# Performance work log

Hardware: AMD Instinct MI355X
Metric: run time of the kernel (lower is better)

## Reference

```python
import jax, jax.numpy as jnp
import numpy as np

V, E, HT, HC = 30000, 300, 256, 256
B, LC, T = 32, 32, 64
NTAG = 9  # output_dim + 2


def lstm_dir(x, lens, Wih, Whh, b, reverse):
    """Variable-length single-direction LSTM (packed-sequence semantics).
    x: [N, T, D], lens: [N] int. Returns outputs [N, T, H] zeroed at pad steps.
    Masked state update keeps h,c frozen at pad steps, so reverse=True starts
    from each sequence's true last element (zeros carry through leading pads).
    """
    N, Tn, _ = x.shape
    H = Whh.shape[1]
    gx = jnp.einsum('ntd,gd->ntg', x, Wih) + b            # [N,T,4H]
    mask = jnp.arange(Tn)[None, :] < lens[:, None]         # [N,T]

    def step(carry, inp):
        h, c = carry
        g_t, m = inp                                       # [N,4H], [N]
        gates = g_t + h @ Whh.T
        i, f, g, o = jnp.split(gates, 4, axis=-1)
        c_new = jax.nn.sigmoid(f) * c + jax.nn.sigmoid(i) * jnp.tanh(g)
        h_new = jax.nn.sigmoid(o) * jnp.tanh(c_new)
        m = m[:, None]
        h2 = jnp.where(m, h_new, h)
        c2 = jnp.where(m, c_new, c)
        return (h2, c2), jnp.where(m, h2, 0.0)

    init = (jnp.zeros((N, H), x.dtype), jnp.zeros((N, H), x.dtype))
    xs = (jnp.swapaxes(gx, 0, 1), mask.T)
    _, ys = jax.lax.scan(step, init, xs, reverse=reverse)
    return jnp.swapaxes(ys, 0, 1)                          # [N,T,H]


def bilstm(x, lens, Wih_f, Whh_f, b_f, Wih_b, Whh_b, b_b):
    hf = lstm_dir(x, lens, Wih_f, Whh_f, b_f, reverse=False)
    hb = lstm_dir(x, lens, Wih_b, Whh_b, b_b, reverse=True)
    return jnp.concatenate([hf, hb], axis=-1)


def setup_inputs() -> dict:
    key = jax.random.key(0)
    ks = jax.random.split(key, 20)
    s = 0.05
    inp = {
        'x': jax.random.randint(ks[0], (B, LC, T), 0, V, dtype=jnp.int32),
        'x_feats': jax.random.normal(ks[1], (B, LC, 64), jnp.float32),
        'x_len': jnp.maximum(jax.random.randint(ks[2], (B,), 0, LC, dtype=jnp.int32), 1),
        'x_chunk_len': jax.random.randint(ks[3], (B, LC), 1, T + 1, dtype=jnp.int32),
        'emb': jax.random.normal(ks[4], (V, E), jnp.float32) * s,
        'tok_Wih_f': jax.random.normal(ks[5], (4 * HT, E), jnp.float32) * s,
        'tok_Whh_f': jax.random.normal(ks[6], (4 * HT, HT), jnp.float32) * s,
        'tok_b_f': jax.random.normal(ks[7], (4 * HT,), jnp.float32) * s,
        'tok_Wih_b': jax.random.normal(ks[8], (4 * HT, E), jnp.float32) * s,
        'tok_Whh_b': jax.random.normal(ks[9], (4 * HT, HT), jnp.float32) * s,
        'tok_b_b': jax.random.normal(ks[10], (4 * HT,), jnp.float32) * s,
        'chk_Wih_f': jax.random.normal(ks[11], (4 * HC, 2 * HT), jnp.float32) * s,
        'chk_Whh_f': jax.random.normal(ks[12], (4 * HC, HC), jnp.float32) * s,
        'chk_b_f': jax.random.normal(ks[13], (4 * HC,), jnp.float32) * s,
        'chk_Wih_b': jax.random.normal(ks[14], (4 * HC, 2 * HT), jnp.float32) * s,
        'chk_Whh_b': jax.random.normal(ks[15], (4 * HC, HC), jnp.float32) * s,
        'chk_b_b': jax.random.normal(ks[16], (4 * HC,), jnp.float32) * s,
        'fc_W': jax.random.normal(ks[17], (NTAG, 2 * HC), jnp.float32) * s,
        'fc_b': jax.random.normal(ks[18], (NTAG,), jnp.float32) * s,
    }
    return inp


def reference(x, x_feats, x_len, x_chunk_len, emb,
              tok_Wih_f, tok_Whh_f, tok_b_f, tok_Wih_b, tok_Whh_b, tok_b_b,
              chk_Wih_f, chk_Whh_f, chk_b_f, chk_Wih_b, chk_Whh_b, chk_b_b,
              fc_W, fc_b):
    b, lc, t = x.shape
    xe = emb[x].reshape(b * lc, t, -1)                     # [B*LC, T, E]
    clens = jnp.clip(x_chunk_len.reshape(-1), 1, t)        # [B*LC]
    h = bilstm(xe, clens, tok_Wih_f, tok_Whh_f, tok_b_f,
               tok_Wih_b, tok_Whh_b, tok_b_b)              # [B*LC, T, 2HT]
    # gather output at last valid timestep (= [fwd final, bwd one-step])
    last = h[jnp.arange(b * lc), clens - 1]                # [B*LC, 2HT]
    chunks = last.reshape(b, lc, -1)                       # [B, LC, 2HT]
    ch = bilstm(chunks, x_len, chk_Wih_f, chk_Whh_f, chk_b_f,
                chk_Wih_b, chk_Whh_b, chk_b_b)             # [B, LC, 2HC]
    # pad_packed(total_length=LC) gives zeros at pad -> fc sees zeros there
    out = ch @ fc_W.T + fc_b                               # [B, LC, NTAG]
    return out
```

## Files before the change

### kernel.cpp

```cpp
#include <hip/hip_runtime.h>


typedef __attribute__((ext_vector_type(8))) short s16x8;
typedef __attribute__((ext_vector_type(4))) float f32x4;
typedef __attribute__((ext_vector_type(2))) unsigned int u32x2;

__device__ __forceinline__ unsigned short f2bf(float f) {
  unsigned u = __builtin_bit_cast(unsigned, f);
  u += 0x7fff + ((u >> 16) & 1);
  return (unsigned short)(u >> 16);
}
__device__ __forceinline__ float bf2f(unsigned short h) {
  unsigned u = ((unsigned)h) << 16;
  return __builtin_bit_cast(float, u);
}
__device__ __forceinline__ float sigm(float x) { return 1.f / (1.f + __expf(-x)); }
__device__ __forceinline__ float tanh_(float x) { return 1.f - 2.f / (__expf(2.f * x) + 1.f); }

union PK8 { s16x8 v; unsigned short u[8]; };

__global__ void prep_weights(const float* __restrict__ wihf, const float* __restrict__ wihb,
                             const float* __restrict__ wcf, const float* __restrict__ wcb,
                             unsigned short* __restrict__ o_wf, unsigned short* __restrict__ o_wb,
                             unsigned short* __restrict__ o_wcf, unsigned short* __restrict__ o_wcb) {
  const int job = blockIdx.y, r = blockIdx.x, tid = threadIdx.x;
  const float* src; unsigned short* dst; int Ks, Kd;
  switch (job) {
    case 0: src = wihf; dst = o_wf;   Ks = 300; Kd = 320; break;
    case 1: src = wihb; dst = o_wb;   Ks = 300; Kd = 320; break;
    case 2: src = wcf;  dst = o_wcf;  Ks = 512; Kd = 512; break;
    default:src = wcb;  dst = o_wcb;  Ks = 512; Kd = 512; break;
  }
  for (int c = tid; c < Kd; c += 256)
    dst[r * Kd + c] = f2bf(c < Ks ? src[r * Ks + c] : 0.f);
}

__global__ __launch_bounds__(256)
void prep_whh_frag(const float* __restrict__ w0, const float* __restrict__ w1,
                   const float* __restrict__ w2,
                   unsigned short* __restrict__ o0, unsigned short* __restrict__ o1,
                   unsigned short* __restrict__ o2) {
  const float* src = blockIdx.y == 0 ? w0 : (blockIdx.y == 1 ? w1 : w2);
  unsigned short* dst = blockIdx.y == 0 ? o0 : (blockIdx.y == 1 ? o1 : o2);
  const int fid = blockIdx.x;
  const int b = fid & 1, g = (fid >> 1) & 3, kt = (fid >> 3) & 7, js = fid >> 6;
  for (int i = threadIdx.x; i < 512; i += 256) {
    const int lane = i >> 3, e = i & 7;
    const int cc = lane & 15, qq = lane >> 4;
    const int row = g * 256 + (js * 2 + b) * 16 + cc;
    const int col = kt * 32 + qq * 8 + e;
    dst[(size_t)fid * 512 + i] = f2bf(src[row * 256 + col]);
  }
}

__global__ void prep_small(const int* __restrict__ x, const int* __restrict__ xcl,
                           int* __restrict__ clens, int* __restrict__ lastv,
                           int* __restrict__ order, int* __restrict__ glen) {
  __shared__ int start[65];
  const int n = threadIdx.x;
  if (n < 65) start[n] = 0;
  __syncthreads();
  int len = xcl[n]; len = len < 1 ? 1 : (len > 64 ? 64 : len);
  clens[n] = len;
  lastv[n] = x[n * 64 + len - 1];
  atomicAdd(&start[len], 1);
  __syncthreads();
  if (n == 0) {
    int acc = 0;
    for (int l = 64; l >= 1; --l) { int h = start[l]; start[l] = acc; acc += h; }
  }
  __syncthreads();
  int pos = atomicAdd(&start[len], 1);
  order[pos] = n;
  __syncthreads();
  if (n < 64) glen[n] = clens[order[n * 16]];
}

__global__ __launch_bounds__(256, 2)
void gemm_bf(const float* __restrict__ A, const int* __restrict__ rowmap,
             int Mrows, int Astride, int Klog, int KP,
             const unsigned short* __restrict__ B, unsigned short* __restrict__ C) {
  __shared__ unsigned short As[128 * 40];
  __shared__ unsigned short Ep[4][64 * 136];
  const int tid = threadIdx.x;
  const int lane = tid & 63, w = tid >> 6;
  const int wrow = w >> 1, wcol = w & 1;
  const int cc = lane & 15, qq = lane >> 4;
  const int m0 = blockIdx.y * 128, n0 = blockIdx.x * 256;

  f32x4 zz = {0.f, 0.f, 0.f, 0.f};
  f32x4 acc[4][8];
#pragma unroll
  for (int i = 0; i < 4; ++i)
#pragma unroll
    for (int j = 0; j < 8; ++j) acc[i][j] = zz;

  const int arow = tid >> 1, ahalf = tid & 1;
  const float* arp = nullptr;
  {
    int av = m0 + arow;
    if (av < Mrows) {
      int amap = rowmap ? rowmap[av] : av;
      arp = A + (long)amap * Astride;
    }
  }

  const int nktiles = KP >> 5;
  for (int kt = 0; kt < nktiles; ++kt) {
    const int k0 = kt << 5;
    __syncthreads();
    {
      const int kb = k0 + ahalf * 16;
      unsigned short hv[16];
      if (arp && kb + 16 <= Klog) {
        const float* p = arp + kb;
#pragma unroll
        for (int i = 0; i < 16; i += 4) {
          f32x4 t = *(const f32x4*)(p + i);
          hv[i] = f2bf(t.x); hv[i + 1] = f2bf(t.y);
          hv[i + 2] = f2bf(t.z); hv[i + 3] = f2bf(t.w);
        }
      } else {
#pragma unroll
        for (int i = 0; i < 16; ++i) {
          float v = (arp && (kb + i) < Klog) ? arp[kb + i] : 0.f;
          hv[i] = f2bf(v);
        }
      }
      PK8 p0, p1;
#pragma unroll
      for (int i = 0; i < 8; ++i) { p0.u[i] = hv[i]; p1.u[i] = hv[8 + i]; }
      *(s16x8*)&As[arow * 40 + ahalf * 16] = p0.v;
      *(s16x8*)&As[arow * 40 + ahalf * 16 + 8] = p1.v;
    }
    __syncthreads();
    s16x8 af[4];
#pragma unroll
    for (int mt = 0; mt < 4; ++mt)
      af[mt] = *(const s16x8*)&As[(wrow * 64 + mt * 16 + cc) * 40 + qq * 8];
#pragma unroll
    for (int nt = 0; nt < 8; ++nt) {
      const unsigned short* bp = B + (long)(n0 + wcol * 128 + nt * 16 + cc) * KP + k0 + qq * 8;
      s16x8 bfr = *(const s16x8*)bp;
#pragma unroll
      for (int mt = 0; mt < 4; ++mt)
        acc[mt][nt] = __builtin_amdgcn_mfma_f32_16x16x32_bf16(af[mt], bfr, acc[mt][nt], 0, 0, 0);
    }
  }
  __syncthreads();
#pragma unroll
  for (int mt = 0; mt < 4; ++mt)
#pragma unroll
    for (int nt = 0; nt < 8; ++nt)
#pragma unroll
      for (int r = 0; r < 4; ++r)
        Ep[w][(mt * 16 + qq * 4 + r) * 136 + nt * 16 + cc] = f2bf(acc[mt][nt][r]);
  __syncthreads();
#pragma unroll
  for (int it = 0; it < 16; ++it) {
    int row = it * 4 + qq;
    s16x8 d = *(const s16x8*)&Ep[w][row * 136 + cc * 8];
    int gm = m0 + wrow * 64 + row;
    int gn = n0 + wcol * 128 + cc * 8;
    if (gm < Mrows) *(s16x8*)&C[(long)gm * 1024 + gn] = d;
  }
}

__global__ void bwd_step(const unsigned short* __restrict__ gxb,
                         const float* __restrict__ bias,
                         float* __restrict__ chunks) {
  const int n = blockIdx.x, j = threadIdx.x;
  const unsigned short* row = gxb + (long)n * 1024;
  float gi = bf2f(row[j]) + bias[j];
  float gg = bf2f(row[512 + j]) + bias[512 + j];
  float go = bf2f(row[768 + j]) + bias[768 + j];
  float cn = sigm(gi) * tanh_(gg);
  chunks[(long)n * 512 + 256 + j] = sigm(go) * tanh_(cn);
}

__global__ __launch_bounds__(256)
void gather_gx(const unsigned short* __restrict__ proj, const int* __restrict__ x,
               const int* __restrict__ order, const int* __restrict__ clens,
               const int* __restrict__ glen, const float* __restrict__ bias,
               unsigned short* __restrict__ gx) {
  const int t = blockIdx.x, p = blockIdx.y, j = threadIdx.x;
  if (t >= glen[p >> 4]) return;
  const int seq = order[p];
  const int len = clens[seq];
  unsigned short* dst = gx + (((size_t)(p >> 4) * 64 + t) * 16 + (p & 15)) * 1024 + j * 4;
  if (t >= len) { u32x2 z = {0u, 0u}; *(u32x2*)dst = z; return; }
  const int tok = x[seq * 64 + t];
  const unsigned short* src = proj + (size_t)tok * 1024 + j;
  unsigned v0 = f2bf(bf2f(src[0]) + bias[j]);
  unsigned v1 = f2bf(bf2f(src[256]) + bias[256 + j]);
  unsigned v2 = f2bf(bf2f(src[512]) + bias[512 + j]);
  unsigned v3 = f2bf(bf2f(src[768]) + bias[768 + j]);
  u32x2 pk = {v0 | (v1 << 16), v2 | (v3 << 16)};
  *(u32x2*)dst = pk;
}

__global__ __launch_bounds__(256)
void repack4(const unsigned short* __restrict__ s0, const unsigned short* __restrict__ s1,
             const float* __restrict__ b0, const float* __restrict__ b1,
             unsigned short* __restrict__ d0, unsigned short* __restrict__ d1) {
  const int r = blockIdx.x, j = threadIdx.x;
  const int m = r >> 5, t = r & 31;
  const int mg = m >> 4, m16 = m & 15;
  const unsigned short* s = (blockIdx.y ? s1 : s0) + (size_t)r * 1024;
  const float* bb = blockIdx.y ? b1 : b0;
  unsigned short* d = (blockIdx.y ? d1 : d0) +
                      (size_t)((mg * 32 + t) * 16 + m16) * 1024 + j * 4;
  unsigned v0 = f2bf(bf2f(s[j]) + bb[j]);
  unsigned v1 = f2bf(bf2f(s[256 + j]) + bb[256 + j]);
  unsigned v2 = f2bf(bf2f(s[512 + j]) + bb[512 + j]);
  unsigned v3 = f2bf(bf2f(s[768 + j]) + bb[768 + j]);
  u32x2 pk = {v0 | (v1 << 16), v2 | (v3 << 16)};
  *(u32x2*)d = pk;
}

__global__ __launch_bounds__(1024, 4)
void tok_fwd(const unsigned short* __restrict__ gx,
             const unsigned short* __restrict__ WhP,
             const int* __restrict__ order,
             const int* __restrict__ clens,
             const int* __restrict__ glen,
             float* __restrict__ chunks) {
  extern __shared__ unsigned short smem[];
  unsigned short* hly = smem;
  unsigned short* ldsW = smem + 4224;
  int* sg = (int*)(smem + 69760);
  int* slen = sg + 16;

  const int tid = threadIdx.x;
  const int lane = tid & 63, w = tid >> 6;
  const int cc = lane & 15, qq = lane >> 4;
  const int gb = blockIdx.x;

  if (tid < 16) {
    int s = order[gb * 16 + tid];
    sg[tid] = s;
    slen[tid] = clens[s];
  }
  for (int i = tid; i < 4224; i += 1024) hly[i] = 0;

  const unsigned short* wgl = WhP + ((size_t)(w >> 1) * 64 + (w & 1)) * 512 + lane * 8;
  {
    unsigned short* ld = ldsW + w * 4096 + lane * 8;
#pragma unroll
    for (int kt = 0; kt < 2; ++kt)
#pragma unroll
      for (int g = 0; g < 4; ++g)
        *(s16x8*)&ld[(kt * 4 + g) * 512] = *(const s16x8*)&wgl[(kt * 8 + g * 2) * 512];
  }
  s16x8 Rw[4];
#pragma unroll
  for (int g = 0; g < 4; ++g) Rw[g] = *(const s16x8*)&wgl[(16 + g * 2) * 512];

  __syncthreads();

  const int maxlen = glen[gb];
  const int j = w * 16 + cc;
  int lenr[4];
#pragma unroll
  for (int r = 0; r < 4; ++r) lenr[r] = slen[qq * 4 + r];

  float cst[4];
#pragma unroll
  for (int r = 0; r < 4; ++r) cst[r] = 0.f;

  const unsigned short* gx0 = gx + (size_t)gb * 64 * 16 * 1024 + j * 4;
  const unsigned short* ldw = ldsW + w * 4096 + lane * 8;
  f32x4 zz = {0.f, 0.f, 0.f, 0.f};

  for (int t = 0; t < maxlen; ++t) {
    __syncthreads();

    u32x2 gxp[4];
#pragma unroll
    for (int r = 0; r < 4; ++r) {
      const int m = qq * 4 + r;
      gxp[r] = *(const u32x2*)(gx0 + ((size_t)t * 16 + m) * 1024);
    }

    f32x4 acc[4];
#pragma unroll
    for (int g = 0; g < 4; ++g) acc[g] = zz;

#pragma unroll
    for (int kt = 0; kt < 2; ++kt) {
      s16x8 a0 = *(const s16x8*)&hly[cc * 264 + kt * 32 + qq * 8];
#pragma unroll
      for (int g = 0; g < 4; ++g) {
        s16x8 bf = *(const s16x8*)&ldw[(kt * 4 + g) * 512];
        acc[g] = __builtin_amdgcn_mfma_f32_16x16x32_bf16(a0, bf, acc[g], 0, 0, 0);
      }
    }
    {
      s16x8 a0 = *(const s16x8*)&hly[cc * 264 + 2 * 32 + qq * 8];
#pragma unroll
      for (int g = 0; g < 4; ++g)
        acc[g] = __builtin_amdgcn_mfma_f32_16x16x32_bf16(a0, Rw[g], acc[g], 0, 0, 0);
    }
#pragma unroll 1
    for (int kt = 3; kt < 8; ++kt) {
      s16x8 Sb[4];
#pragma unroll
      for (int g = 0; g < 4; ++g)
        Sb[g] = *(const s16x8*)&wgl[(kt * 8 + g * 2) * 512];
      s16x8 a0 = *(const s16x8*)&hly[cc * 264 + kt * 32 + qq * 8];
#pragma unroll
      for (int g = 0; g < 4; ++g)
        acc[g] = __builtin_amdgcn_mfma_f32_16x16x32_bf16(a0, Sb[g], acc[g], 0, 0, 0);
    }

    __syncthreads();

#pragma unroll
    for (int r = 0; r < 4; ++r) {
      const int m = qq * 4 + r;
      const u32x2 pk = gxp[r];
      float gi = acc[0][r] + bf2f((unsigned short)(pk.x & 0xffff));
      float gf = acc[1][r] + bf2f((unsigned short)(pk.x >> 16));
      float gg = acc[2][r] + bf2f((unsigned short)(pk.y & 0xffff));
      float go = acc[3][r] + bf2f((unsigned short)(pk.y >> 16));
      if (t < lenr[r]) {
        float cn = sigm(gf) * cst[r] + sigm(gi) * tanh_(gg);
        cst[r] = cn;
        float hn = sigm(go) * tanh_(cn);
        hly[m * 264 + j] = f2bf(hn);
      }
    }
  }

  __syncthreads();
#pragma unroll
  for (int r = 0; r < 4; ++r) {
    const int m = qq * 4 + r;
    chunks[(size_t)sg[m] * 512 + j] = bf2f(hly[m * 264 + j]);
  }
}

__global__ __launch_bounds__(1024, 4)
void chunk_rec(const unsigned short* __restrict__ gxf,
               const unsigned short* __restrict__ gxb,
               const unsigned short* __restrict__ WhPf,
               const unsigned short* __restrict__ WhPb,
               const int* __restrict__ xlen,
               unsigned short* __restrict__ ch) {
  extern __shared__ unsigned short smem[];
  unsigned short* hly = smem;
  unsigned short* ldsW = smem + 4224;

  const int tid = threadIdx.x;
  const int lane = tid & 63, w = tid >> 6;
  const int cc = lane & 15, qq = lane >> 4;
  const int dir = blockIdx.x & 1, mg = blockIdx.x >> 1;
  const unsigned short* gx = (dir ? gxb : gxf) + (size_t)mg * 32 * 16 * 1024;
  const unsigned short* WhP = dir ? WhPb : WhPf;

  for (int i = tid; i < 4224; i += 1024) hly[i] = 0;

  const unsigned short* wgl = WhP + ((size_t)(w >> 1) * 64 + (w & 1)) * 512 + lane * 8;
  {
    unsigned short* ld = ldsW + w * 4096 + lane * 8;
#pragma unroll
    for (int kt = 0; kt < 2; ++kt)
#pragma unroll
      for (int g = 0; g < 4; ++g)
        *(s16x8*)&ld[(kt * 4 + g) * 512] = *(const s16x8*)&wgl[(kt * 8 + g * 2) * 512];
  }
  s16x8 Rw[4];
#pragma unroll
  for (int g = 0; g < 4; ++g) Rw[g] = *(const s16x8*)&wgl[(16 + g * 2) * 512];

  __syncthreads();

  const int j = w * 16 + cc;
  int lenr[4];
#pragma unroll
  for (int r = 0; r < 4; ++r) {
    int L = xlen[mg * 16 + qq * 4 + r];
    lenr[r] = L > 32 ? 32 : L;
  }

  float cst[4];
#pragma unroll
  for (int r = 0; r < 4; ++r) cst[r] = 0.f;

  const unsigned short* ldw = ldsW + w * 4096 + lane * 8;
  f32x4 zz = {0.f, 0.f, 0.f, 0.f};

  for (int tt = 0; tt < 32; ++tt) {
    const int t = dir ? (31 - tt) : tt;

    __syncthreads();

    u32x2 gxp[4];
#pragma unroll
    for (int r = 0; r < 4; ++r) {
      const int m = qq * 4 + r;
      gxp[r] = *(const u32x2*)(gx + ((size_t)t * 16 + m) * 1024 + j * 4);
    }

    f32x4 acc[4];
#pragma unroll
    for (int g = 0; g < 4; ++g) acc[g] = zz;

#pragma unroll
    for (int kt = 0; kt < 2; ++kt) {
      s16x8 a0 = *(const s16x8*)&hly[cc * 264 + kt * 32 + qq * 8];
#pragma unroll
      for (int g = 0; g < 4; ++g) {
        s16x8 bf = *(const s16x8*)&ldw[(kt * 4 + g) * 512];
        acc[g] = __builtin_amdgcn_mfma_f32_16x16x32_bf16(a0, bf, acc[g], 0, 0, 0);
      }
    }
    {
      s16x8 a0 = *(const s16x8*)&hly[cc * 264 + 2 * 32 + qq * 8];
#pragma unroll
      for (int g = 0; g < 4; ++g)
        acc[g] = __builtin_amdgcn_mfma_f32_16x16x32_bf16(a0, Rw[g], acc[g], 0, 0, 0);
    }
#pragma unroll 1
    for (int kt = 3; kt < 8; ++kt) {
      s16x8 Sb[4];
#pragma unroll
      for (int g = 0; g < 4; ++g)
        Sb[g] = *(const s16x8*)&wgl[(kt * 8 + g * 2) * 512];
      s16x8 a0 = *(const s16x8*)&hly[cc * 264 + kt * 32 + qq * 8];
#pragma unroll
      for (int g = 0; g < 4; ++g)
        acc[g] = __builtin_amdgcn_mfma_f32_16x16x32_bf16(a0, Sb[g], acc[g], 0, 0, 0);
    }

    __syncthreads();

#pragma unroll
    for (int r = 0; r < 4; ++r) {
      const int m = qq * 4 + r;
      const u32x2 pk = gxp[r];
      float gi = acc[0][r] + bf2f((unsigned short)(pk.x & 0xffff));
      float gf = acc[1][r] + bf2f((unsigned short)(pk.x >> 16));
      float gg = acc[2][r] + bf2f((unsigned short)(pk.y & 0xffff));
      float go = acc[3][r] + bf2f((unsigned short)(pk.y >> 16));
      unsigned short hb16 = 0;
      if (t < lenr[r]) {
        float cn = sigm(gf) * cst[r] + sigm(gi) * tanh_(gg);
        cst[r] = cn;
        float hn = sigm(go) * tanh_(cn);
        hb16 = f2bf(hn);
        hly[m * 264 + j] = hb16;
      }
      ch[(size_t)((mg * 16 + m) * 32 + t) * 512 + dir * 256 + j] = hb16;
    }
  }
}

__global__ __launch_bounds__(64)
void fc_kernel(const unsigned short* __restrict__ ch, const float* __restrict__ W,
               const float* __restrict__ bfc, float* __restrict__ out) {
  const int n = blockIdx.x, lane = threadIdx.x;
  float xv[8];
  const unsigned short* cp = ch + (long)n * 512 + lane * 8;
#pragma unroll
  for (int i = 0; i < 8; ++i) xv[i] = bf2f(cp[i]);
  float s[9];
#pragma unroll
  for (int k = 0; k < 9; ++k) {
    const float* wr = W + k * 512 + lane * 8;
    float t = 0.f;
#pragma unroll
    for (int i = 0; i < 8; ++i) t += xv[i] * wr[i];
    s[k] = t;
  }
#pragma unroll
  for (int off = 32; off; off >>= 1)
#pragma unroll
    for (int k = 0; k < 9; ++k) s[k] += __shfl_down(s[k], off, 64);
  if (lane == 0) {
#pragma unroll
    for (int k = 0; k < 9; ++k) out[n * 9 + k] = s[k] + bfc[k];
  }
}

extern "C" void kernel_launch(void* const* d_in, const int* in_sizes, int n_in,
                              void* d_out, int out_size, void* d_ws, size_t ws_size,
                              hipStream_t stream) {
  const int*   x           = (const int*)d_in[0];
  const int*   x_len       = (const int*)d_in[2];
  const int*   x_chunk_len = (const int*)d_in[3];
  const float* emb         = (const float*)d_in[4];
  const float* tok_Wih_f   = (const float*)d_in[5];
  const float* tok_Whh_f   = (const float*)d_in[6];
  const float* tok_b_f     = (const float*)d_in[7];
  const float* tok_Wih_b   = (const float*)d_in[8];
  const float* tok_b_b     = (const float*)d_in[10];
  const float* chk_Wih_f   = (const float*)d_in[11];
  const float* chk_Whh_f   = (const float*)d_in[12];
  const float* chk_b_f     = (const float*)d_in[13];
  const float* chk_Wih_b   = (const float*)d_in[14];
  const float* chk_Whh_b   = (const float*)d_in[15];
  const float* chk_b_b     = (const float*)d_in[16];
  const float* fc_W        = (const float*)d_in[17];
  const float* fc_b        = (const float*)d_in[18];
  float* out = (float*)d_out;

  char* ws = (char*)d_ws;
  size_t off = 0;
  auto alloc = [&](size_t bytes) -> void* {
    void* p = ws + off;
    off += (bytes + 255) & ~(size_t)255;
    return p;
  };
  unsigned short* Wf   = (unsigned short*)alloc((size_t)1024 * 320 * 2);
  unsigned short* Wb   = (unsigned short*)alloc((size_t)1024 * 320 * 2);
  unsigned short* Wcf  = (unsigned short*)alloc((size_t)1024 * 512 * 2);
  unsigned short* Wcb  = (unsigned short*)alloc((size_t)1024 * 512 * 2);
  unsigned short* WhPtok=(unsigned short*)alloc((size_t)512 * 512 * 2);
  unsigned short* WhPcf= (unsigned short*)alloc((size_t)512 * 512 * 2);
  unsigned short* WhPcb= (unsigned short*)alloc((size_t)512 * 512 * 2);
  unsigned short* proj = (unsigned short*)alloc((size_t)30000 * 1024 * 2);
  unsigned short* gxbb = (unsigned short*)alloc((size_t)1024 * 1024 * 2);
  unsigned short* gxcf = (unsigned short*)alloc((size_t)1024 * 1024 * 2);
  unsigned short* gxcb = (unsigned short*)alloc((size_t)1024 * 1024 * 2);
  unsigned short* gxcfp= (unsigned short*)alloc((size_t)1024 * 1024 * 2);
  unsigned short* gxcbp= (unsigned short*)alloc((size_t)1024 * 1024 * 2);
  float*          chunks = (float*)alloc((size_t)1024 * 512 * 4);
  unsigned short* cho  = (unsigned short*)alloc((size_t)1024 * 512 * 2);
  unsigned short* gxs  = (unsigned short*)alloc((size_t)1024 * 64 * 1024 * 2);
  int* clens = (int*)alloc(1024 * 4);
  int* lastv = (int*)alloc(1024 * 4);
  int* order = (int*)alloc(1024 * 4);
  int* glen  = (int*)alloc(64 * 4);

  hipFuncSetAttribute((const void*)tok_fwd,
                      hipFuncAttributeMaxDynamicSharedMemorySize, 139776);
  hipFuncSetAttribute((const void*)chunk_rec,
                      hipFuncAttributeMaxDynamicSharedMemorySize, 139520);

  prep_weights<<<dim3(1024, 4), 256, 0, stream>>>(
      tok_Wih_f, tok_Wih_b, chk_Wih_f, chk_Wih_b, Wf, Wb, Wcf, Wcb);
  prep_whh_frag<<<dim3(512, 3), 256, 0, stream>>>(
      tok_Whh_f, chk_Whh_f, chk_Whh_b, WhPtok, WhPcf, WhPcb);
  prep_small<<<1, 1024, 0, stream>>>(x, x_chunk_len, clens, lastv, order, glen);

  gemm_bf<<<dim3(4, 235), 256, 0, stream>>>(emb, nullptr, 30000, 300, 300, 320, Wf, proj);
  gemm_bf<<<dim3(4, 8), 256, 0, stream>>>(emb, lastv, 1024, 300, 300, 320, Wb, gxbb);
  bwd_step<<<1024, 256, 0, stream>>>(gxbb, tok_b_b, chunks);
  gather_gx<<<dim3(64, 1024), 256, 0, stream>>>(proj, x, order, clens, glen, tok_b_f, gxs);
  tok_fwd<<<64, 1024, 139776, stream>>>(gxs, WhPtok, order, clens, glen, chunks);
  gemm_bf<<<dim3(4, 8), 256, 0, stream>>>(chunks, nullptr, 1024, 512, 512, 512, Wcf, gxcf);
  gemm_bf<<<dim3(4, 8), 256, 0, stream>>>(chunks, nullptr, 1024, 512, 512, 512, Wcb, gxcb);
  repack4<<<dim3(1024, 2), 256, 0, stream>>>(gxcf, gxcb, chk_b_f, chk_b_b, gxcfp, gxcbp);
  chunk_rec<<<4, 1024, 139520, stream>>>(gxcfp, gxcbp, WhPcf, WhPcb, x_len, cho);
  fc_kernel<<<1024, 64, 0, stream>>>(cho, fc_W, fc_b, out);
}
```

Measured before the change: 908.3 us.

## Double-buffer hidden state in LDS and pipeline recurrent weight loads

The recurrent kernels now keep two hidden-state buffers in LDS, alternating by step. This removes one block-wide barrier per timestep. The weight sections streamed from global memory are double-buffered in registers, so the next section (and the first section of the next step) is loaded while the current one feeds the MFMAs. This costs extra LDS and register pressure. Masked rows leave stale data in the inactive buffer, which is handled by reading the final state from the buffer selected by sequence-length parity.

```diff
diff --git a/kernel.cpp b/kernel.cpp
--- a/kernel.cpp
+++ b/kernel.cpp
@@ -18,6 +18,20 @@
 __device__ __forceinline__ float tanh_(float x) { return 1.f - 2.f / (__expf(2.f * x) + 1.f); }
 
 union PK8 { s16x8 v; unsigned short u[8]; };
+
+#define LOADSEC(buf, kt) { _Pragma("unroll") \
+  for (int g = 0; g < 4; ++g) buf[g] = *(const s16x8*)&wgl[((kt) * 8 + g * 2) * 512]; }
+
+#define MFMASEC(kt, buf) { \
+  s16x8 a0 = *(const s16x8*)&hc[cc * 264 + (kt) * 32 + qq * 8]; \
+  _Pragma("unroll") for (int g = 0; g < 4; ++g) \
+    acc[g] = __builtin_amdgcn_mfma_f32_16x16x32_bf16(a0, buf[g], acc[g], 0, 0, 0); }
+
+#define MFMALDS(kt) { \
+  s16x8 a0 = *(const s16x8*)&hc[cc * 264 + (kt) * 32 + qq * 8]; \
+  _Pragma("unroll") for (int g = 0; g < 4; ++g) { \
+    s16x8 bf = *(const s16x8*)&ldw[((kt) * 4 + g) * 512]; \
+    acc[g] = __builtin_amdgcn_mfma_f32_16x16x32_bf16(a0, bf, acc[g], 0, 0, 0); } }
 
 __global__ void prep_weights(const float* __restrict__ wihf, const float* __restrict__ wihb,
                              const float* __restrict__ wcf, const float* __restrict__ wcb,
@@ -227,8 +241,8 @@
              float* __restrict__ chunks) {
   extern __shared__ unsigned short smem[];
   unsigned short* hly = smem;
-  unsigned short* ldsW = smem + 4224;
-  int* sg = (int*)(smem + 69760);
+  unsigned short* ldsW = smem + 8448;
+  int* sg = (int*)(smem + 73984);
   int* slen = sg + 16;
 
   const int tid = threadIdx.x;
@@ -241,7 +255,7 @@
     sg[tid] = s;
     slen[tid] = clens[s];
   }
-  for (int i = tid; i < 4224; i += 1024) hly[i] = 0;
+  for (int i = tid; i < 8448; i += 1024) hly[i] = 0;
 
   const unsigned short* wgl = WhP + ((size_t)(w >> 1) * 64 + (w & 1)) * 512 + lane * 8;
   {
@@ -252,9 +266,6 @@
       for (int g = 0; g < 4; ++g)
         *(s16x8*)&ld[(kt * 4 + g) * 512] = *(const s16x8*)&wgl[(kt * 8 + g * 2) * 512];
   }
-  s16x8 Rw[4];
-#pragma unroll
-  for (int g = 0; g < 4; ++g) Rw[g] = *(const s16x8*)&wgl[(16 + g * 2) * 512];
 
   __syncthreads();
 
@@ -272,8 +283,12 @@
   const unsigned short* ldw = ldsW + w * 4096 + lane * 8;
   f32x4 zz = {0.f, 0.f, 0.f, 0.f};
 
+  s16x8 Sa[4], Sb[4];
+  LOADSEC(Sa, 2)
+
   for (int t = 0; t < maxlen; ++t) {
-    __syncthreads();
+    const unsigned short* hc = hly + (t & 1) * 4224;
+    unsigned short* hn = hly + ((t + 1) & 1) * 4224;
 
     u32x2 gxp[4];
 #pragma unroll
@@ -286,34 +301,14 @@
 #pragma unroll
     for (int g = 0; g < 4; ++g) acc[g] = zz;
 
-#pragma unroll
-    for (int kt = 0; kt < 2; ++kt) {
-      s16x8 a0 = *(const s16x8*)&hly[cc * 264 + kt * 32 + qq * 8];
-#pragma unroll
-      for (int g = 0; g < 4; ++g) {
-        s16x8 bf = *(const s16x8*)&ldw[(kt * 4 + g) * 512];
-        acc[g] = __builtin_amdgcn_mfma_f32_16x16x32_bf16(a0, bf, acc[g], 0, 0, 0);
-      }
-    }
-    {
-      s16x8 a0 = *(const s16x8*)&hly[cc * 264 + 2 * 32 + qq * 8];
-#pragma unroll
-      for (int g = 0; g < 4; ++g)
-        acc[g] = __builtin_amdgcn_mfma_f32_16x16x32_bf16(a0, Rw[g], acc[g], 0, 0, 0);
-    }
-#pragma unroll 1
-    for (int kt = 3; kt < 8; ++kt) {
-      s16x8 Sb[4];
-#pragma unroll
-      for (int g = 0; g < 4; ++g)
-        Sb[g] = *(const s16x8*)&wgl[(kt * 8 + g * 2) * 512];
-      s16x8 a0 = *(const s16x8*)&hly[cc * 264 + kt * 32 + qq * 8];
-#pragma unroll
-      for (int g = 0; g < 4; ++g)
-        acc[g] = __builtin_amdgcn_mfma_f32_16x16x32_bf16(a0, Sb[g], acc[g], 0, 0, 0);
-    }
-
-    __syncthreads();
+    MFMALDS(0)
+    MFMALDS(1)
+    LOADSEC(Sb, 3)  MFMASEC(2, Sa)
+    LOADSEC(Sa, 4)  MFMASEC(3, Sb)
+    LOADSEC(Sb, 5)  MFMASEC(4, Sa)
+    LOADSEC(Sa, 6)  MFMASEC(5, Sb)
+    LOADSEC(Sb, 7)  MFMASEC(6, Sa)
+    LOADSEC(Sa, 2)  MFMASEC(7, Sb)
 
 #pragma unroll
     for (int r = 0; r < 4; ++r) {
@@ -326,17 +321,18 @@
       if (t < lenr[r]) {
         float cn = sigm(gf) * cst[r] + sigm(gi) * tanh_(gg);
         cst[r] = cn;
-        float hn = sigm(go) * tanh_(cn);
-        hly[m * 264 + j] = f2bf(hn);
+        float hn_ = sigm(go) * tanh_(cn);
+        hn[m * 264 + j] = f2bf(hn_);
       }
     }
-  }
-
-  __syncthreads();
+
+    __syncthreads();
+  }
+
 #pragma unroll
   for (int r = 0; r < 4; ++r) {
     const int m = qq * 4 + r;
-    chunks[(size_t)sg[m] * 512 + j] = bf2f(hly[m * 264 + j]);
+    chunks[(size_t)sg[m] * 512 + j] = bf2f(hly[(lenr[r] & 1) * 4224 + m * 264 + j]);
   }
 }
 
@@ -349,7 +345,7 @@
                unsigned short* __restrict__ ch) {
   extern __shared__ unsigned short smem[];
   unsigned short* hly = smem;
-  unsigned short* ldsW = smem + 4224;
+  unsigned short* ldsW = smem + 8448;
 
   const int tid = threadIdx.x;
   const int lane = tid & 63, w = tid >> 6;
@@ -358,7 +354,7 @@
   const unsigned short* gx = (dir ? gxb : gxf) + (size_t)mg * 32 * 16 * 1024;
   const unsigned short* WhP = dir ? WhPb : WhPf;
 
-  for (int i = tid; i < 4224; i += 1024) hly[i] = 0;
+  for (int i = tid; i < 8448; i += 1024) hly[i] = 0;
 
   const unsigned short* wgl = WhP + ((size_t)(w >> 1) * 64 + (w & 1)) * 512 + lane * 8;
   {
@@ -369,9 +365,6 @@
       for (int g = 0; g < 4; ++g)
         *(s16x8*)&ld[(kt * 4 + g) * 512] = *(const s16x8*)&wgl[(kt * 8 + g * 2) * 512];
   }
-  s16x8 Rw[4];
-#pragma unroll
-  for (int g = 0; g < 4; ++g) Rw[g] = *(const s16x8*)&wgl[(16 + g * 2) * 512];
 
   __syncthreads();
 
@@ -390,10 +383,13 @@
   const unsigned short* ldw = ldsW + w * 4096 + lane * 8;
   f32x4 zz = {0.f, 0.f, 0.f, 0.f};
 
+  s16x8 Sa[4], Sb[4];
+  LOADSEC(Sa, 2)
+
   for (int tt = 0; tt < 32; ++tt) {
     const int t = dir ? (31 - tt) : tt;
-
-    __syncthreads();
+    const unsigned short* hc = hly + (tt & 1) * 4224;
+    unsigned short* hn = hly + ((tt + 1) & 1) * 4224;
 
     u32x2 gxp[4];
 #pragma unroll
@@ -406,34 +402,14 @@
 #pragma unroll
     for (int g = 0; g < 4; ++g) acc[g] = zz;
 
-#pragma unroll
-    for (int kt = 0; kt < 2; ++kt) {
-      s16x8 a0 = *(const s16x8*)&hly[cc * 264 + kt * 32 + qq * 8];
-#pragma unroll
-      for (int g = 0; g < 4; ++g) {
-        s16x8 bf = *(const s16x8*)&ldw[(kt * 4 + g) * 512];
-        acc[g] = __builtin_amdgcn_mfma_f32_16x16x32_bf16(a0, bf, acc[g], 0, 0, 0);
-      }
-    }
-    {
-      s16x8 a0 = *(const s16x8*)&hly[cc * 264 + 2 * 32 + qq * 8];
-#pragma unroll
-      for (int g = 0; g < 4; ++g)
-        acc[g] = __builtin_amdgcn_mfma_f32_16x16x32_bf16(a0, Rw[g], acc[g], 0, 0, 0);
-    }
-#pragma unroll 1
-    for (int kt = 3; kt < 8; ++kt) {
-      s16x8 Sb[4];
-#pragma unroll
-      for (int g = 0; g < 4; ++g)
-        Sb[g] = *(const s16x8*)&wgl[(kt * 8 + g * 2) * 512];
-      s16x8 a0 = *(const s16x8*)&hly[cc * 264 + kt * 32 + qq * 8];
-#pragma unroll
-      for (int g = 0; g < 4; ++g)
-        acc[g] = __builtin_amdgcn_mfma_f32_16x16x32_bf16(a0, Sb[g], acc[g], 0, 0, 0);
-    }
-
-    __syncthreads();
+    MFMALDS(0)
+    MFMALDS(1)
+    LOADSEC(Sb, 3)  MFMASEC(2, Sa)
+    LOADSEC(Sa, 4)  MFMASEC(3, Sb)
+    LOADSEC(Sb, 5)  MFMASEC(4, Sa)
+    LOADSEC(Sa, 6)  MFMASEC(5, Sb)
+    LOADSEC(Sb, 7)  MFMASEC(6, Sa)
+    LOADSEC(Sa, 2)  MFMASEC(7, Sb)
 
 #pragma unroll
     for (int r = 0; r < 4; ++r) {
@@ -447,12 +423,14 @@
       if (t < lenr[r]) {
         float cn = sigm(gf) * cst[r] + sigm(gi) * tanh_(gg);
         cst[r] = cn;
-        float hn = sigm(go) * tanh_(cn);
-        hb16 = f2bf(hn);
-        hly[m * 264 + j] = hb16;
+        float hv = sigm(go) * tanh_(cn);
+        hb16 = f2bf(hv);
+        hn[m * 264 + j] = hb16;
       }
       ch[(size_t)((mg * 16 + m) * 32 + t) * 512 + dir * 256 + j] = hb16;
     }
+
+    __syncthreads();
   }
 }
 
@@ -534,9 +512,9 @@
   int* glen  = (int*)alloc(64 * 4);
 
   hipFuncSetAttribute((const void*)tok_fwd,
-                      hipFuncAttributeMaxDynamicSharedMemorySize, 139776);
+                      hipFuncAttributeMaxDynamicSharedMemorySize, 148096);
   hipFuncSetAttribute((const void*)chunk_rec,
-                      hipFuncAttributeMaxDynamicSharedMemorySize, 139520);
+                      hipFuncAttributeMaxDynamicSharedMemorySize, 147968);
 
   prep_weights<<<dim3(1024, 4), 256, 0, stream>>>(
       tok_Wih_f, tok_Wih_b, chk_Wih_f, chk_Wih_b, Wf, Wb, Wcf, Wcb);
@@ -548,10 +526,10 @@
   gemm_bf<<<dim3(4, 8), 256, 0, stream>>>(emb, lastv, 1024, 300, 300, 320, Wb, gxbb);
   bwd_step<<<1024, 256, 0, stream>>>(gxbb, tok_b_b, chunks);
   gather_gx<<<dim3(64, 1024), 256, 0, stream>>>(proj, x, order, clens, glen, tok_b_f, gxs);
-  tok_fwd<<<64, 1024, 139776, stream>>>(gxs, WhPtok, order, clens, glen, chunks);
+  tok_fwd<<<64, 1024, 148096, stream>>>(gxs, WhPtok, order, clens, glen, chunks);
   gemm_bf<<<dim3(4, 8), 256, 0, stream>>>(chunks, nullptr, 1024, 512, 512, 512, Wcf, gxcf);
   gemm_bf<<<dim3(4, 8), 256, 0, stream>>>(chunks, nullptr, 1024, 512, 512, 512, Wcb, gxcb);
   repack4<<<dim3(1024, 2), 256, 0, stream>>>(gxcf, gxcb, chk_b_f, chk_b_b, gxcfp, gxcbp);
-  chunk_rec<<<4, 1024, 139520, stream>>>(gxcfp, gxcbp, WhPcf, WhPcb, x_len, cho);
+  chunk_rec<<<4, 1024, 147968, stream>>>(gxcfp, gxcbp, WhPcf, WhPcb, x_len, cho);
   fc_kernel<<<1024, 64, 0, stream>>>(cho, fc_W, fc_b, out);
 }
```

Result: no change. 917.9 us (+1.1%).
